# Kernel tuning notes

Measured on AMD Instinct MI355X. Metric: run time of the kernel, lower is better.

Reference implementation:

```python
import jax, jax.numpy as jnp
import numpy as np

EPS = 1e-5
L = 256
CHANNELS = 256


def setup_inputs() -> dict:
    key = jax.random.key(0)
    ks = jax.random.split(key, 7)
    B, C, D, H, W = 2, 256, 48, 48, 48
    x = jax.random.normal(ks[0], (B, C, D, H, W), dtype=jnp.float32)
    # Conv1d(kernel=1) weights: [out_channels, in_channels], plus bias.
    s = 1.0 / np.sqrt(C)
    Wq = jax.random.uniform(ks[1], (CHANNELS, C), jnp.float32, -s, s)
    bq = jax.random.uniform(ks[2], (CHANNELS,), jnp.float32, -s, s)
    Wk = jax.random.uniform(ks[3], (CHANNELS, C), jnp.float32, -s, s)
    bk = jax.random.uniform(ks[4], (CHANNELS,), jnp.float32, -s, s)
    Wv = jax.random.uniform(ks[5], (CHANNELS, C), jnp.float32, -s, s)
    bv = jax.random.uniform(ks[6], (CHANNELS,), jnp.float32, -s, s)
    outer = jnp.eye(L, dtype=jnp.float32)  # learned, init = identity
    return {"x": x, "Wq": Wq, "bq": bq, "Wk": Wk, "bk": bk, "Wv": Wv, "bv": bv, "outer": outer}


def reference(x, Wq, bq, Wk, bk, Wv, bv, outer):
    B, C, D, H, W = x.shape
    N = D * H * W
    # InstanceNorm3d (affine=False): normalize per (B, C) over spatial dims, biased var.
    xf = x.reshape(B, C, N)
    mean = jnp.mean(xf, axis=-1, keepdims=True)
    var = jnp.mean(jnp.square(xf - mean), axis=-1, keepdims=True)
    xn = (xf - mean) * jax.lax.rsqrt(var + EPS)  # [B, C, N]
    # 1x1 Conv1d projections == GEMM over channel dim.
    q = jnp.einsum('oc,bcn->bon', Wq, xn) + bq[None, :, None]
    k = jnp.einsum('oc,bcn->bon', Wk, xn) + bk[None, :, None]
    v = jnp.einsum('oc,bcn->bon', Wv, xn) + bv[None, :, None]
    # Channel attention: scores [B, C, C]; scale applied AFTER softmax.
    scores = jnp.einsum('bcn,bdn->bcd', q, k)
    atten = jax.nn.softmax(scores, axis=-1) / jnp.sqrt(jnp.float32(CHANNELS))
    atten = atten + (outer / jnp.sqrt(jnp.float32(L)))[None, :, :]
    out = jnp.einsum('bcd,bdn->bcn', atten, v)
    # Residual is to the NORMALIZED x (x was reassigned in the original forward).
    return (out + xn).reshape(B, C, D, H, W)
```

## Files before the change

### kernel.cpp

```cpp
#include <hip/hip_runtime.h>
#include <hip/hip_bf16.h>

#define B_ 2
#define C_ 256
#define N_ 110592
#define CN_ ((size_t)C_ * N_)
#define NCK_ 108
#define T_ 16

typedef __attribute__((ext_vector_type(4))) float f32x4;
typedef __attribute__((ext_vector_type(8))) short bf16x8;
typedef __attribute__((ext_vector_type(4))) short bf16x4;

__device__ __forceinline__ short f2bf(float f) {
    union { float f; unsigned u; } v; v.f = f;
    unsigned r = (v.u + 0x7fffu + ((v.u >> 16) & 1u)) >> 16;
    return (short)(r & 0xffffu);
}

__device__ __forceinline__ void gload16(const short* g, short* l) {
    __builtin_amdgcn_global_load_lds(
        (const __attribute__((address_space(1))) void*)g,
        (__attribute__((address_space(3))) void*)l, 16, 0, 0);
}

__global__ __launch_bounds__(1024, 4) void k_gram(
        const float* __restrict__ x, float* __restrict__ part,
        float* __restrict__ rspart, short* __restrict__ xf, int wxf) {
    __shared__ short Xs[2 * 256 * 72];
    __shared__ float rs_s[256];
    const int t = threadIdx.x, lane = t & 63, wave = t >> 6;
    const int chunk = blockIdx.x, b = blockIdx.y;
    const int k0 = chunk * (T_ * 64);
    const int f4 = t & 15;
    const int crow = t >> 4;
    const int cw0 = (wave & 3) * 64, dw0 = (wave >> 2) * 64;
    const int r16 = lane & 15, g16 = lane >> 4;
    const float* xb = x + (size_t)b * CN_;
    short* xfb = xf + (size_t)b * CN_;

    f32x4 acc[4][4];
#pragma unroll
    for (int i = 0; i < 4; ++i)
#pragma unroll
        for (int j = 0; j < 4; ++j) acc[i][j] = f32x4{0.f, 0.f, 0.f, 0.f};
    float rs[4] = {0.f, 0.f, 0.f, 0.f};

    f32x4 va[4];
#pragma unroll
    for (int q = 0; q < 4; ++q)
        va[q] = *(const f32x4*)(xb + (size_t)(q * 64 + crow) * N_ + k0 + f4 * 4);

    for (int tt = 0; tt < T_; ++tt) {
        const int buf = (tt & 1) * 18432;
#pragma unroll
        for (int q = 0; q < 4; ++q) {
            f32x4 v = va[q];
            rs[q] += (v.x + v.y) + (v.z + v.w);
            bf16x4 h;
            h.x = f2bf(v.x); h.y = f2bf(v.y); h.z = f2bf(v.z); h.w = f2bf(v.w);
            *(bf16x4*)(Xs + buf + (q * 64 + crow) * 72 + f4 * 4) = h;
        }
        __syncthreads();
        if (tt + 1 < T_) {
#pragma unroll
            for (int q = 0; q < 4; ++q)
                va[q] = *(const f32x4*)(xb + (size_t)(q * 64 + crow) * N_ +
                                        k0 + (tt + 1) * 64 + f4 * 4);
        }
        if (wxf) {
            const int kglob0 = k0 + tt * 64;
#pragma unroll
            for (int i2 = 0; i2 < 2; ++i2) {
                int s = i2 * 1024 + t;
                int kg = s >> 6, nn = s & 63;
                bf16x8 h;
#pragma unroll
                for (int j = 0; j < 8; ++j)
                    h[j] = Xs[buf + (kg * 8 + j) * 72 + nn];
                *(bf16x8*)(xfb + ((size_t)kg * N_ + kglob0 + nn) * 8) = h;
            }
        }
#pragma unroll
        for (int k2 = 0; k2 < 2; ++k2) {
            bf16x8 afr[4];
#pragma unroll
            for (int ct = 0; ct < 4; ++ct)
                afr[ct] = *(const bf16x8*)(Xs + buf + (cw0 + ct * 16 + r16) * 72 +
                                           (k2 * 4 + g16) * 8);
#pragma unroll
            for (int dt = 0; dt < 4; ++dt) {
                bf16x8 bfr = *(const bf16x8*)(Xs + buf + (dw0 + dt * 16 + r16) * 72 +
                                              (k2 * 4 + g16) * 8);
#pragma unroll
                for (int ct = 0; ct < 4; ++ct)
                    acc[ct][dt] = __builtin_amdgcn_mfma_f32_16x16x32_bf16(
                        afr[ct], bfr, acc[ct][dt], 0, 0, 0);
            }
        }
    }

#pragma unroll
    for (int q = 0; q < 4; ++q) {
        float r = rs[q];
        r += __shfl_xor(r, 1);
        r += __shfl_xor(r, 2);
        r += __shfl_xor(r, 4);
        r += __shfl_xor(r, 8);
        if ((t & 15) == 0) rs_s[q * 64 + crow] = r;
    }
    __syncthreads();
    if (t < 256) rspart[((size_t)b * NCK_ + chunk) * C_ + t] = rs_s[t];

    float* pp = part + ((size_t)b * NCK_ + chunk) * (C_ * C_);
#pragma unroll
    for (int ct = 0; ct < 4; ++ct)
#pragma unroll
        for (int dt = 0; dt < 4; ++dt) {
            int d = dw0 + dt * 16 + r16;
#pragma unroll
            for (int rr = 0; rr < 4; ++rr) {
                int c = cw0 + ct * 16 + g16 * 4 + rr;
                pp[(size_t)c * C_ + d] = acc[ct][dt][rr];
            }
        }
}

__global__ void k_reduce(const float* __restrict__ part, const float* __restrict__ rspart,
                         float* __restrict__ Graw, float* __restrict__ mean,
                         float* __restrict__ rsig) {
    __shared__ float diag_s;
    __shared__ float red[256];
    int bid = blockIdx.x;
    int b = bid >> 8, c = bid & 255;
    int d = threadIdx.x;
    float s = 0.f;
    for (int p = 0; p < NCK_; ++p)
        s += part[(((size_t)b * NCK_ + p) * (C_ * C_)) + (size_t)c * C_ + d];
    Graw[((size_t)b * C_ + c) * C_ + d] = s;
    if (d == c) diag_s = s;
    float rsum = 0.f;
    for (int p = d; p < NCK_; p += 256)
        rsum += rspart[((size_t)b * NCK_ + p) * C_ + c];
    red[d] = rsum;
    __syncthreads();
    if (d < 128) red[d] += red[d + 128];
    __syncthreads();
    if (d < 64) red[d] += red[d + 64];
    __syncthreads();
    if (d == 0) {
        float tot = 0.f;
#pragma unroll
        for (int i = 0; i < 64; ++i) tot += red[i];
        float m = tot / (float)N_;
        float var = diag_s / (float)N_ - m * m;
        mean[b * C_ + c] = m;
        rsig[b * C_ + c] = rsqrtf(var + 1e-5f);
    }
}

__global__ void k_gemm1(const float* __restrict__ Wq, const float* __restrict__ Graw,
                        const float* __restrict__ mean, const float* __restrict__ rsig,
                        float* __restrict__ P) {
    int bid = blockIdx.x; int b = bid >> 8, c = bid & 255; int d = threadIdx.x;
    const float* G = Graw + (size_t)b * C_ * C_;
    const float* mb = mean + b * C_;
    const float* rb = rsig + b * C_;
    float md = mb[d], rd = rb[d];
    float a1 = 0.f, a2 = 0.f;
    for (int e = 0; e < C_; ++e) {
        float w = Wq[(size_t)c * C_ + e] * rb[e];
        a1 += w * G[(size_t)e * C_ + d];
        a2 += w * mb[e];
    }
    P[((size_t)b * C_ + c) * C_ + d] = rd * a1 - (float)N_ * md * rd * a2;
}

__global__ void k_attn(const float* __restrict__ P, const float* __restrict__ Wk,
                       const float* __restrict__ bq, const float* __restrict__ bk,
                       const float* __restrict__ outer, float* __restrict__ atten) {
    __shared__ float Pr_s[256];
    __shared__ float red[8];
    int bid = blockIdx.x; int b = bid >> 8, c = bid & 255; int d = threadIdx.x;
    int lane = d & 63, w = d >> 6;
    Pr_s[d] = P[((size_t)b * C_ + c) * C_ + d];
    __syncthreads();
    float a = 0.f;
#pragma unroll 4
    for (int e4 = 0; e4 < 64; ++e4) {
        f32x4 wv = *(const f32x4*)(Wk + (size_t)d * C_ + e4 * 4);
        f32x4 pv = *(const f32x4*)(Pr_s + e4 * 4);
        a += wv.x * pv.x + wv.y * pv.y + wv.z * pv.z + wv.w * pv.w;
    }
    float v = a + (float)N_ * bq[c] * bk[d];
    float m = v;
    for (int off = 32; off; off >>= 1) m = fmaxf(m, __shfl_xor(m, off));
    if (lane == 0) red[w] = m;
    __syncthreads();
    m = fmaxf(fmaxf(red[0], red[1]), fmaxf(red[2], red[3]));
    float e = __expf(v - m);
    float s = e;
    for (int off = 32; off; off >>= 1) s += __shfl_xor(s, off);
    if (lane == 0) red[4 + w] = s;
    __syncthreads();
    s = red[4] + red[5] + red[6] + red[7];
    atten[((size_t)b * C_ + c) * C_ + d] = e / (s * 16.f) + outer[(size_t)c * C_ + d] * 0.0625f;
}

__global__ void k_gemm3(const float* __restrict__ atten, const float* __restrict__ Wv,
                        const float* __restrict__ bv, const float* __restrict__ mean,
                        const float* __restrict__ rsig, short* __restrict__ Abf,
                        float* __restrict__ beta) {
    __shared__ float red[4];
    int bid = blockIdx.x; int b = bid >> 8, c = bid & 255; int g = threadIdx.x;
    int lane = g & 63, w = g >> 6;
    const float* at = atten + ((size_t)b * C_ + c) * C_;
    float a = 0.f;
    for (int d = 0; d < C_; ++d)
        a += at[d] * Wv[(size_t)d * C_ + g];
    float Ag = (a + ((g == c) ? 1.f : 0.f)) * rsig[b * C_ + g];
    Abf[(size_t)b * C_ * C_ + ((size_t)(g >> 3) * C_ + c) * 8 + (g & 7)] = f2bf(Ag);
    float u = at[g] * bv[g] - Ag * mean[b * C_ + g];
    for (int off = 32; off; off >>= 1) u += __shfl_xor(u, off);
    if (lane == 0) red[w] = u;
    __syncthreads();
    if (g == 0) beta[b * C_ + c] = red[0] + red[1] + red[2] + red[3];
}

__global__ __launch_bounds__(512, 4) void k_out2(
        const short* __restrict__ xf, const short* __restrict__ Abf,
        const float* __restrict__ beta, float* __restrict__ out) {
    __shared__ short Xt[2 * 8192];
    __shared__ float Wb[8 * 32 * 33];
    const int t = threadIdx.x, lane = t & 63, wave = t >> 6;
    const int nb = blockIdx.x, b = blockIdx.y;
    const int col = lane & 15, g16 = lane >> 4;
    const int cw0 = wave * 32;
    const int r8 = lane >> 3, s8 = lane & 7;
    const int n_blk = nb * 256;
    const short* Ab = Abf + (size_t)b * C_ * C_;
    const short* xfb = xf + (size_t)b * CN_;
    float* ob = out + (size_t)b * CN_;
    float* wl = Wb + wave * (32 * 33);

    bf16x8 Af[2][8];
#pragma unroll
    for (int ct = 0; ct < 2; ++ct)
#pragma unroll
        for (int ks = 0; ks < 8; ++ks)
            Af[ct][ks] = *(const bf16x8*)(Ab +
                ((size_t)((ks * 4 + g16) * 256 + cw0 + ct * 16 + col)) * 8);
    float bet[4];
#pragma unroll
    for (int j = 0; j < 4; ++j) bet[j] = beta[b * C_ + cw0 + j * 8 + r8];

#define STAGE(BUF, N0)                                                        \
    {                                                                         \
        _Pragma("unroll")                                                     \
        for (int r = 0; r < 2; ++r) {                                         \
            int s = r * 512 + t;                                              \
            int kg = s >> 5, nsl = s & 31;                                    \
            int nn = nsl ^ (kg & 3);                                          \
            gload16(xfb + ((size_t)kg * N_ + (N0) + nn) * 8,                  \
                    Xt + (BUF) * 8192 + s * 8);                               \
        }                                                                     \
    }

    STAGE(0, n_blk)
    __syncthreads();

    for (int it = 0; it < 8; ++it) {
        const int cur = it & 1;
        if (it + 1 < 8) STAGE(cur ^ 1, n_blk + (it + 1) * 32)
        const int n0 = n_blk + it * 32;

        f32x4 acc[2][2];
#pragma unroll
        for (int i = 0; i < 2; ++i) {
            acc[i][0] = f32x4{0.f, 0.f, 0.f, 0.f};
            acc[i][1] = f32x4{0.f, 0.f, 0.f, 0.f};
        }
#pragma unroll
        for (int ks = 0; ks < 8; ++ks) {
            const int kg = ks * 4 + g16;
            bf16x8 x0 = *(const bf16x8*)(Xt + cur * 8192 +
                                         (kg * 32 + (col ^ (kg & 3))) * 8);
            bf16x8 x1 = *(const bf16x8*)(Xt + cur * 8192 +
                                         (kg * 32 + ((16 + col) ^ (kg & 3))) * 8);
            acc[0][0] = __builtin_amdgcn_mfma_f32_16x16x32_bf16(Af[0][ks], x0, acc[0][0], 0, 0, 0);
            acc[1][0] = __builtin_amdgcn_mfma_f32_16x16x32_bf16(Af[1][ks], x0, acc[1][0], 0, 0, 0);
            acc[0][1] = __builtin_amdgcn_mfma_f32_16x16x32_bf16(Af[0][ks], x1, acc[0][1], 0, 0, 0);
            acc[1][1] = __builtin_amdgcn_mfma_f32_16x16x32_bf16(Af[1][ks], x1, acc[1][1], 0, 0, 0);
        }
#pragma unroll
        for (int ct = 0; ct < 2; ++ct)
#pragma unroll
            for (int nt = 0; nt < 2; ++nt)
#pragma unroll
                for (int rr = 0; rr < 4; ++rr)
                    wl[(ct * 16 + g16 * 4 + rr) * 33 + nt * 16 + col] = acc[ct][nt][rr];
#pragma unroll
        for (int j = 0; j < 4; ++j) {
            f32x4 v = *(const f32x4*)(wl + (j * 8 + r8) * 33 + s8 * 4);
            float bb = bet[j];
            v.x += bb; v.y += bb; v.z += bb; v.w += bb;
            *(f32x4*)(ob + (size_t)(cw0 + j * 8 + r8) * N_ + n0 + s8 * 4) = v;
        }
        __syncthreads();
    }
#undef STAGE
}

__global__ __launch_bounds__(512) void k_out_f32(
        const float* __restrict__ x, const short* __restrict__ Abf,
        const float* __restrict__ beta, float* __restrict__ out) {
    __shared__ float beta_s[256];
    const int t = threadIdx.x, lane = t & 63, wave = t >> 6;
    const int nb = blockIdx.x, b = blockIdx.y;
    const int col = lane & 15, g16 = lane >> 4;
    const int n_w = nb * 256 + wave * 32;
    if (t < 256) beta_s[t] = beta[b * C_ + t];
    __syncthreads();
    const short* Ab = Abf + (size_t)b * C_ * C_;
    const float* xb = x + (size_t)b * CN_;
    float* ob = out + (size_t)b * CN_;

    f32x4 acc[16][2];
#pragma unroll
    for (int i = 0; i < 16; ++i) {
        acc[i][0] = f32x4{0.f, 0.f, 0.f, 0.f};
        acc[i][1] = f32x4{0.f, 0.f, 0.f, 0.f};
    }
    float pf[2][16];
#define XL(KS, NT, J) xb[(size_t)((KS)*32 + g16 * 8 + (J)) * N_ + n_w + (NT)*16 + col]
#pragma unroll
    for (int j = 0; j < 8; ++j) { pf[0][j] = XL(0, 0, j); pf[0][8 + j] = XL(0, 1, j); }
#pragma unroll
    for (int ks = 0; ks < 8; ++ks) {
        if (ks + 1 < 8) {
#pragma unroll
            for (int j = 0; j < 8; ++j) {
                pf[(ks + 1) & 1][j] = XL(ks + 1, 0, j);
                pf[(ks + 1) & 1][8 + j] = XL(ks + 1, 1, j);
            }
        }
        bf16x8 xa, xv;
#pragma unroll
        for (int j = 0; j < 8; ++j) {
            xa[j] = f2bf(pf[ks & 1][j]);
            xv[j] = f2bf(pf[ks & 1][8 + j]);
        }
#pragma unroll
        for (int ct = 0; ct < 16; ++ct) {
            bf16x8 afr = *(const bf16x8*)(Ab + ((size_t)((ks * 4 + g16) * 256 + ct * 16 + col)) * 8);
            acc[ct][0] = __builtin_amdgcn_mfma_f32_16x16x32_bf16(afr, xa, acc[ct][0], 0, 0, 0);
            acc[ct][1] = __builtin_amdgcn_mfma_f32_16x16x32_bf16(afr, xv, acc[ct][1], 0, 0, 0);
        }
    }
#undef XL
#pragma unroll
    for (int ct = 0; ct < 16; ++ct)
#pragma unroll
        for (int nt = 0; nt < 2; ++nt) {
            int n = n_w + nt * 16 + col;
#pragma unroll
            for (int rr = 0; rr < 4; ++rr) {
                int c = ct * 16 + g16 * 4 + rr;
                ob[(size_t)c * N_ + n] = acc[ct][nt][rr] + beta_s[c];
            }
        }
}

extern "C" void kernel_launch(void* const* d_in, const int* in_sizes, int n_in,
                              void* d_out, int out_size, void* d_ws, size_t ws_size,
                              hipStream_t stream) {
    (void)in_sizes; (void)n_in; (void)out_size;
    const float* x     = (const float*)d_in[0];
    const float* Wq    = (const float*)d_in[1];
    const float* bq    = (const float*)d_in[2];
    const float* Wk    = (const float*)d_in[3];
    const float* bk    = (const float*)d_in[4];
    const float* Wv    = (const float*)d_in[5];
    const float* bv    = (const float*)d_in[6];
    const float* outer = (const float*)d_in[7];
    float* out = (float*)d_out;

    char* w = (char*)d_ws;
    float* mean   = (float*)(w + 0);
    float* rsig   = (float*)(w + 2048);
    float* beta   = (float*)(w + 4096);
    float* rspart = (float*)(w + 8192);
    float* Graw   = (float*)(w + 262144);
    float* P      = (float*)(w + 786432);
    float* atten  = (float*)(w + 1310720);
    short* Abf    = (short*)(w + 1835008);
    const size_t fixed = 2097152;
    const size_t part_bytes = (size_t)NCK_ * B_ * C_ * C_ * 4;
    const size_t xf_bytes = (size_t)B_ * CN_ * 2;
    float* part = (float*)(w + fixed);
    short* xf   = (short*)(w + fixed + part_bytes);

    const bool big = ws_size >= fixed + part_bytes + xf_bytes;

    k_gram  <<<dim3(NCK_, B_), 1024, 0, stream>>>(x, part, rspart, xf, big ? 1 : 0);
    k_reduce<<<dim3(B_ * C_), 256, 0, stream>>>(part, rspart, Graw, mean, rsig);
    k_gemm1 <<<dim3(B_ * C_), C_, 0, stream>>>(Wq, Graw, mean, rsig, P);
    k_attn  <<<dim3(B_ * C_), C_, 0, stream>>>(P, Wk, bq, bk, outer, atten);
    k_gemm3 <<<dim3(B_ * C_), C_, 0, stream>>>(atten, Wv, bv, mean, rsig, Abf, beta);
    if (big) {
        k_out2  <<<dim3(N_ / 256, B_), 512, 0, stream>>>(xf, Abf, beta, out);
    } else {
        k_out_f32<<<dim3(N_ / 256, B_), 512, 0, stream>>>(x, Abf, beta, out);
    }
}
```

Measured before the change: 230.7 us.

## Split gram kernel across output column halves with 512-thread blocks

The Gram kernel now runs two blocks per chunk, each computing half of the 256x256 output columns with 512 threads, so each block reloads and converts the full x tile. Only the first half writes row sums and the bf16 copy of x. The register prefetch double-buffering of the next tile is removed in favour of loading the current tile directly. This doubles block count for better occupancy but also doubles global reads of x and the bf16 conversion work.

```diff
diff --git a/kernel.cpp b/kernel.cpp
--- a/kernel.cpp
+++ b/kernel.cpp
@@ -24,74 +24,70 @@
         (__attribute__((address_space(3))) void*)l, 16, 0, 0);
 }
 
-__global__ __launch_bounds__(1024, 4) void k_gram(
+__global__ __launch_bounds__(512, 4) void k_gram(
         const float* __restrict__ x, float* __restrict__ part,
         float* __restrict__ rspart, short* __restrict__ xf, int wxf) {
     __shared__ short Xs[2 * 256 * 72];
     __shared__ float rs_s[256];
     const int t = threadIdx.x, lane = t & 63, wave = t >> 6;
-    const int chunk = blockIdx.x, b = blockIdx.y;
+    const int chunk = blockIdx.x, dh = blockIdx.y, b = blockIdx.z;
     const int k0 = chunk * (T_ * 64);
     const int f4 = t & 15;
     const int crow = t >> 4;
-    const int cw0 = (wave & 3) * 64, dw0 = (wave >> 2) * 64;
+    const int cw0 = (wave & 3) * 64;
+    const int dw0 = dh * 128 + (wave >> 2) * 64;
     const int r16 = lane & 15, g16 = lane >> 4;
     const float* xb = x + (size_t)b * CN_;
     short* xfb = xf + (size_t)b * CN_;
+    const bool doaux = (dh == 0);
 
     f32x4 acc[4][4];
 #pragma unroll
     for (int i = 0; i < 4; ++i)
 #pragma unroll
         for (int j = 0; j < 4; ++j) acc[i][j] = f32x4{0.f, 0.f, 0.f, 0.f};
-    float rs[4] = {0.f, 0.f, 0.f, 0.f};
-
-    f32x4 va[4];
-#pragma unroll
-    for (int q = 0; q < 4; ++q)
-        va[q] = *(const f32x4*)(xb + (size_t)(q * 64 + crow) * N_ + k0 + f4 * 4);
+    float rs[8] = {0.f, 0.f, 0.f, 0.f, 0.f, 0.f, 0.f, 0.f};
 
     for (int tt = 0; tt < T_; ++tt) {
         const int buf = (tt & 1) * 18432;
-#pragma unroll
-        for (int q = 0; q < 4; ++q) {
-            f32x4 v = va[q];
-            rs[q] += (v.x + v.y) + (v.z + v.w);
+        f32x4 v[8];
+#pragma unroll
+        for (int p = 0; p < 8; ++p)
+            v[p] = *(const f32x4*)(xb + (size_t)(p * 32 + crow) * N_ +
+                                   k0 + tt * 64 + f4 * 4);
+#pragma unroll
+        for (int p = 0; p < 8; ++p) {
+            if (doaux) rs[p] += (v[p].x + v[p].y) + (v[p].z + v[p].w);
             bf16x4 h;
-            h.x = f2bf(v.x); h.y = f2bf(v.y); h.z = f2bf(v.z); h.w = f2bf(v.w);
-            *(bf16x4*)(Xs + buf + (q * 64 + crow) * 72 + f4 * 4) = h;
+            h.x = f2bf(v[p].x); h.y = f2bf(v[p].y);
+            h.z = f2bf(v[p].z); h.w = f2bf(v[p].w);
+            *(bf16x4*)(Xs + buf + (p * 32 + crow) * 72 + f4 * 4) = h;
         }
         __syncthreads();
-        if (tt + 1 < T_) {
-#pragma unroll
-            for (int q = 0; q < 4; ++q)
-                va[q] = *(const f32x4*)(xb + (size_t)(q * 64 + crow) * N_ +
-                                        k0 + (tt + 1) * 64 + f4 * 4);
-        }
-        if (wxf) {
-            const int kglob0 = k0 + tt * 64;
-#pragma unroll
-            for (int i2 = 0; i2 < 2; ++i2) {
-                int s = i2 * 1024 + t;
+        if (doaux && wxf) {
+            const int ng0 = k0 + tt * 64;
+#pragma unroll
+            for (int it = 0; it < 4; ++it) {
+                int s = it * 512 + t;
                 int kg = s >> 6, nn = s & 63;
                 bf16x8 h;
 #pragma unroll
                 for (int j = 0; j < 8; ++j)
                     h[j] = Xs[buf + (kg * 8 + j) * 72 + nn];
-                *(bf16x8*)(xfb + ((size_t)kg * N_ + kglob0 + nn) * 8) = h;
+                *(bf16x8*)(xfb + ((size_t)kg * N_ + ng0 + nn) * 8) = h;
             }
         }
 #pragma unroll
-        for (int k2 = 0; k2 < 2; ++k2) {
+        for (int kst = 0; kst < 2; ++kst) {
             bf16x8 afr[4];
 #pragma unroll
             for (int ct = 0; ct < 4; ++ct)
                 afr[ct] = *(const bf16x8*)(Xs + buf + (cw0 + ct * 16 + r16) * 72 +
-                                           (k2 * 4 + g16) * 8);
+                                           kst * 32 + g16 * 8);
 #pragma unroll
             for (int dt = 0; dt < 4; ++dt) {
                 bf16x8 bfr = *(const bf16x8*)(Xs + buf + (dw0 + dt * 16 + r16) * 72 +
-                                              (k2 * 4 + g16) * 8);
+                                              kst * 32 + g16 * 8);
 #pragma unroll
                 for (int ct = 0; ct < 4; ++ct)
                     acc[ct][dt] = __builtin_amdgcn_mfma_f32_16x16x32_bf16(
@@ -100,17 +96,19 @@
         }
     }
 
-#pragma unroll
-    for (int q = 0; q < 4; ++q) {
-        float r = rs[q];
-        r += __shfl_xor(r, 1);
-        r += __shfl_xor(r, 2);
-        r += __shfl_xor(r, 4);
-        r += __shfl_xor(r, 8);
-        if ((t & 15) == 0) rs_s[q * 64 + crow] = r;
-    }
-    __syncthreads();
-    if (t < 256) rspart[((size_t)b * NCK_ + chunk) * C_ + t] = rs_s[t];
+    if (doaux) {
+#pragma unroll
+        for (int p = 0; p < 8; ++p) {
+            float r = rs[p];
+            r += __shfl_xor(r, 1);
+            r += __shfl_xor(r, 2);
+            r += __shfl_xor(r, 4);
+            r += __shfl_xor(r, 8);
+            if ((t & 15) == 0) rs_s[p * 32 + crow] = r;
+        }
+        __syncthreads();
+        if (t < 256) rspart[((size_t)b * NCK_ + chunk) * C_ + t] = rs_s[t];
+    }
 
     float* pp = part + ((size_t)b * NCK_ + chunk) * (C_ * C_);
 #pragma unroll
@@ -402,7 +400,7 @@
 
     const bool big = ws_size >= fixed + part_bytes + xf_bytes;
 
-    k_gram  <<<dim3(NCK_, B_), 1024, 0, stream>>>(x, part, rspart, xf, big ? 1 : 0);
+    k_gram  <<<dim3(NCK_, 2, B_), 512, 0, stream>>>(x, part, rspart, xf, big ? 1 : 0);
     k_reduce<<<dim3(B_ * C_), 256, 0, stream>>>(part, rspart, Graw, mean, rsig);
     k_gemm1 <<<dim3(B_ * C_), C_, 0, stream>>>(Wq, Graw, mean, rsig, P);
     k_attn  <<<dim3(B_ * C_), C_, 0, stream>>>(P, Wk, bq, bk, outer, atten);
```

Result: slower. 285.1 us (+23.6%).

## Pipeline Gram kernel loads via async global-to-LDS triple buffering with smaller tiles

Applied to the files above, without the earlier changes.

Reworks the Gram kernel so fp32 input tiles are copied straight into LDS with global_load_lds into a triple-buffered ring, prefetched two steps ahead, instead of being loaded through registers. Each step now covers 32 columns rather than 64, and the chunk count rises from 108 to 128 so more blocks run. A separate bf16 conversion pass is added per step, with an XOR swizzle to avoid bank conflicts. Workspace offsets are enlarged to fit the extra partial sums. The cost is more barriers per element, smaller MFMA K per barrier, and a larger partial-sum reduction.

```diff
diff --git a/kernel.cpp b/kernel.cpp
--- a/kernel.cpp
+++ b/kernel.cpp
@@ -5,8 +5,9 @@
 #define C_ 256
 #define N_ 110592
 #define CN_ ((size_t)C_ * N_)
-#define NCK_ 108
-#define T_ 16
+#define NCK_ 128
+#define TW_ 32
+#define T_ 27
 
 typedef __attribute__((ext_vector_type(4))) float f32x4;
 typedef __attribute__((ext_vector_type(8))) short bf16x8;
@@ -18,97 +19,104 @@
     return (short)(r & 0xffffu);
 }
 
-__device__ __forceinline__ void gload16(const short* g, short* l) {
+__device__ __forceinline__ void gload16f(const float* g, float* l) {
     __builtin_amdgcn_global_load_lds(
         (const __attribute__((address_space(1))) void*)g,
         (__attribute__((address_space(3))) void*)l, 16, 0, 0);
 }
 
+__device__ __forceinline__ void gload16s(const short* g, short* l) {
+    __builtin_amdgcn_global_load_lds(
+        (const __attribute__((address_space(1))) void*)g,
+        (__attribute__((address_space(3))) void*)l, 16, 0, 0);
+}
+
 __global__ __launch_bounds__(1024, 4) void k_gram(
         const float* __restrict__ x, float* __restrict__ part,
         float* __restrict__ rspart, short* __restrict__ xf, int wxf) {
-    __shared__ short Xs[2 * 256 * 72];
+    __shared__ float Xf[3 * 8192];
+    __shared__ short Xb[256 * 40];
     __shared__ float rs_s[256];
     const int t = threadIdx.x, lane = t & 63, wave = t >> 6;
     const int chunk = blockIdx.x, b = blockIdx.y;
-    const int k0 = chunk * (T_ * 64);
-    const int f4 = t & 15;
-    const int crow = t >> 4;
+    const int k0 = chunk * (T_ * TW_);
     const int cw0 = (wave & 3) * 64, dw0 = (wave >> 2) * 64;
     const int r16 = lane & 15, g16 = lane >> 4;
     const float* xb = x + (size_t)b * CN_;
     short* xfb = xf + (size_t)b * CN_;
 
+    const int s_row = t >> 3;
+    const int g_src = (t & 7) ^ (s_row & 7);
+    const int rp_r = t >> 2, rp_q = t & 3;
+    const int rp_g0 = (2 * rp_q) ^ (rp_r & 7);
+    const int em_cg = t >> 5, em_nn = t & 31;
+
     f32x4 acc[4][4];
 #pragma unroll
     for (int i = 0; i < 4; ++i)
 #pragma unroll
         for (int j = 0; j < 4; ++j) acc[i][j] = f32x4{0.f, 0.f, 0.f, 0.f};
-    float rs[4] = {0.f, 0.f, 0.f, 0.f};
-
-    f32x4 va[4];
-#pragma unroll
-    for (int q = 0; q < 4; ++q)
-        va[q] = *(const f32x4*)(xb + (size_t)(q * 64 + crow) * N_ + k0 + f4 * 4);
-
+    float rs = 0.f;
+
+#define GSTAGE(TT, BB)                                                        \
+    {                                                                         \
+        const float* gsrc = xb + k0 + (TT) * TW_ + g_src * 4;                 \
+        float* ldst = Xf + (BB) * 8192;                                       \
+        gload16f(gsrc + (size_t)s_row * N_, ldst + t * 4);                    \
+        gload16f(gsrc + (size_t)(s_row + 128) * N_, ldst + (t + 1024) * 4);   \
+    }
+
+    GSTAGE(0, 0)
+    GSTAGE(1, 1)
+
+    int bb = 0;
     for (int tt = 0; tt < T_; ++tt) {
-        const int buf = (tt & 1) * 18432;
-#pragma unroll
-        for (int q = 0; q < 4; ++q) {
-            f32x4 v = va[q];
-            rs[q] += (v.x + v.y) + (v.z + v.w);
-            bf16x4 h;
-            h.x = f2bf(v.x); h.y = f2bf(v.y); h.z = f2bf(v.z); h.w = f2bf(v.w);
-            *(bf16x4*)(Xs + buf + (q * 64 + crow) * 72 + f4 * 4) = h;
-        }
-        __syncthreads();
-        if (tt + 1 < T_) {
-#pragma unroll
-            for (int q = 0; q < 4; ++q)
-                va[q] = *(const f32x4*)(xb + (size_t)(q * 64 + crow) * N_ +
-                                        k0 + (tt + 1) * 64 + f4 * 4);
-        }
-        if (wxf) {
-            const int kglob0 = k0 + tt * 64;
-#pragma unroll
-            for (int i2 = 0; i2 < 2; ++i2) {
-                int s = i2 * 1024 + t;
-                int kg = s >> 6, nn = s & 63;
-                bf16x8 h;
-#pragma unroll
-                for (int j = 0; j < 8; ++j)
-                    h[j] = Xs[buf + (kg * 8 + j) * 72 + nn];
-                *(bf16x8*)(xfb + ((size_t)kg * N_ + kglob0 + nn) * 8) = h;
-            }
-        }
-#pragma unroll
-        for (int k2 = 0; k2 < 2; ++k2) {
+        asm volatile("s_waitcnt vmcnt(2)" ::: "memory");
+        __builtin_amdgcn_s_barrier();
+        if (tt + 2 < T_) {
+            int bn = bb + 2; if (bn >= 3) bn -= 3;
+            GSTAGE(tt + 2, bn)
+        }
+        {
+            const float* src = Xf + bb * 8192 + rp_r * 32;
+            f32x4 a = *(const f32x4*)(src + rp_g0 * 4);
+            f32x4 c = *(const f32x4*)(src + (rp_g0 ^ 1) * 4);
+            rs += ((a.x + a.y) + (a.z + a.w)) + ((c.x + c.y) + (c.z + c.w));
+            bf16x8 h;
+            h[0] = f2bf(a.x); h[1] = f2bf(a.y); h[2] = f2bf(a.z); h[3] = f2bf(a.w);
+            h[4] = f2bf(c.x); h[5] = f2bf(c.y); h[6] = f2bf(c.z); h[7] = f2bf(c.w);
+            *(bf16x8*)(Xb + rp_r * 40 + rp_q * 8) = h;
+        }
+        asm volatile("s_waitcnt lgkmcnt(0)" ::: "memory");
+        __builtin_amdgcn_s_barrier();
+        {
             bf16x8 afr[4];
 #pragma unroll
             for (int ct = 0; ct < 4; ++ct)
-                afr[ct] = *(const bf16x8*)(Xs + buf + (cw0 + ct * 16 + r16) * 72 +
-                                           (k2 * 4 + g16) * 8);
+                afr[ct] = *(const bf16x8*)(Xb + (cw0 + ct * 16 + r16) * 40 + g16 * 8);
 #pragma unroll
             for (int dt = 0; dt < 4; ++dt) {
-                bf16x8 bfr = *(const bf16x8*)(Xs + buf + (dw0 + dt * 16 + r16) * 72 +
-                                              (k2 * 4 + g16) * 8);
+                bf16x8 bfr = *(const bf16x8*)(Xb + (dw0 + dt * 16 + r16) * 40 + g16 * 8);
 #pragma unroll
                 for (int ct = 0; ct < 4; ++ct)
                     acc[ct][dt] = __builtin_amdgcn_mfma_f32_16x16x32_bf16(
                         afr[ct], bfr, acc[ct][dt], 0, 0, 0);
             }
         }
-    }
-
-#pragma unroll
-    for (int q = 0; q < 4; ++q) {
-        float r = rs[q];
-        r += __shfl_xor(r, 1);
-        r += __shfl_xor(r, 2);
-        r += __shfl_xor(r, 4);
-        r += __shfl_xor(r, 8);
-        if ((t & 15) == 0) rs_s[q * 64 + crow] = r;
-    }
+        if (wxf) {
+            bf16x8 h;
+#pragma unroll
+            for (int j = 0; j < 8; ++j)
+                h[j] = Xb[(em_cg * 8 + j) * 40 + em_nn];
+            *(bf16x8*)(xfb + ((size_t)em_cg * N_ + k0 + tt * TW_ + em_nn) * 8) = h;
+        }
+        ++bb; if (bb >= 3) bb -= 3;
+    }
+#undef GSTAGE
+
+    rs += __shfl_xor(rs, 1);
+    rs += __shfl_xor(rs, 2);
+    if (rp_q == 0) rs_s[rp_r] = rs;
     __syncthreads();
     if (t < 256) rspart[((size_t)b * NCK_ + chunk) * C_ + t] = rs_s[t];
 
@@ -261,8 +269,8 @@
             int s = r * 512 + t;                                              \
             int kg = s >> 5, nsl = s & 31;                                    \
             int nn = nsl ^ (kg & 3);                                          \
-            gload16(xfb + ((size_t)kg * N_ + (N0) + nn) * 8,                  \
-                    Xt + (BUF) * 8192 + s * 8);                               \
+            gload16s(xfb + ((size_t)kg * N_ + (N0) + nn) * 8,                 \
+                     Xt + (BUF) * 8192 + s * 8);                              \
         }                                                                     \
     }
 
@@ -390,11 +398,11 @@
     float* rsig   = (float*)(w + 2048);
     float* beta   = (float*)(w + 4096);
     float* rspart = (float*)(w + 8192);
-    float* Graw   = (float*)(w + 262144);
-    float* P      = (float*)(w + 786432);
-    float* atten  = (float*)(w + 1310720);
-    short* Abf    = (short*)(w + 1835008);
-    const size_t fixed = 2097152;
+    float* Graw   = (float*)(w + 270336);
+    float* P      = (float*)(w + 794624);
+    float* atten  = (float*)(w + 1318912);
+    short* Abf    = (short*)(w + 1843200);
+    const size_t fixed = 2105344;
     const size_t part_bytes = (size_t)NCK_ * B_ * C_ * C_ * 4;
     const size_t xf_bytes = (size_t)B_ * CN_ * 2;
     float* part = (float*)(w + fixed);
```

After: 229.0 us. No clear change (-0.7%).
